# Performance work log

Hardware: AMD Instinct MI355X
Metric: run time of the kernel (lower is better)

## Reference

```python
import math
import jax, jax.numpy as jnp
import numpy as np

B, S, D, H = 4, 2048, 1024, 16
HD = D // H

def setup_inputs() -> dict:
    key = jax.random.key(0)
    ks = jax.random.split(key, 8)
    std = 1.0 / math.sqrt(D)
    return {
        "query": jax.random.normal(ks[0], (B, S, D), jnp.float32),
        "key":   jax.random.normal(ks[1], (B, S, D), jnp.float32),
        "value": jax.random.normal(ks[2], (B, S, D), jnp.float32),
        "Wq": jax.random.normal(ks[3], (D, D), jnp.float32) * std,
        "Wk": jax.random.normal(ks[4], (D, D), jnp.float32) * std,
        "Wv": jax.random.normal(ks[5], (D, D), jnp.float32) * std,
        "Wo": jax.random.normal(ks[6], (D, D), jnp.float32) * std,
        "bo": jnp.zeros((D,), jnp.float32),
    }

def reference(query, key, value, Wq, Wk, Wv, Wo, bo):
    # Projections (bias-free, as in source)
    Q = query @ Wq   # [B,S,D]
    K = key   @ Wk
    V = value @ Wv
    # Split heads: [B,S,D] -> [B,H,S,HD]
    def split(x):
        return x.reshape(B, S, H, HD).transpose(0, 2, 1, 3)
    Qh, Kh, Vh = split(Q), split(K), split(V)
    # NOTE: source scales by sqrt(d_model), not sqrt(head_dim)
    scale = 1.0 / math.sqrt(D)
    scores = jnp.einsum("bhqd,bhkd->bhqk", Qh, Kh) * scale  # [B,H,S,S]
    attn = jax.nn.softmax(scores, axis=-1)
    out = jnp.einsum("bhqk,bhkd->bhqd", attn, Vh)           # [B,H,S,HD]
    out = out.transpose(0, 2, 1, 3).reshape(B, S, D)
    return out @ Wo + bo
```

## Files before the change

kernel.cpp:

```cpp
#include <hip/hip_runtime.h>
#include <hip/hip_bf16.h>
#include <stdint.h>

typedef short bf16x8 __attribute__((ext_vector_type(8)));
typedef float f32x4 __attribute__((ext_vector_type(4)));
typedef float f32x16 __attribute__((ext_vector_type(16)));
typedef unsigned int uint2v __attribute__((ext_vector_type(2)));
typedef unsigned short u16;

static const size_t SD = (size_t)8192 * 1024;
static const size_t DD = (size_t)1024 * 1024;

__device__ __forceinline__ u16 f2bf(float f) {
  unsigned int u = __builtin_bit_cast(unsigned int, f);
  u += 0x7fffu + ((u >> 16) & 1u);
  return (u16)(u >> 16);
}

__device__ __forceinline__ unsigned int cvt_pk_bf16(float a, float b) {
  unsigned int r;
  asm("v_cvt_pk_bf16_f32 %0, %1, %2" : "=v"(r) : "v"(a), "v"(b));
  return r;
}

__device__ __forceinline__ float exp2_hw(float x) {
  float r;
  asm("v_exp_f32 %0, %1" : "=v"(r) : "v"(x));
  return r;
}

__device__ __forceinline__ void async_copy16(const void* g, void* l) {
  __builtin_amdgcn_global_load_lds(
      (const __attribute__((address_space(1))) unsigned int*)g,
      (__attribute__((address_space(3))) unsigned int*)l, 16, 0, 0);
}

__device__ __forceinline__ void wb2() {
  asm volatile("s_waitcnt vmcnt(2)\ns_barrier" ::: "memory");
  __builtin_amdgcn_sched_barrier(0);
}
__device__ __forceinline__ void wb0() {
  asm volatile("s_waitcnt vmcnt(0)\ns_barrier" ::: "memory");
  __builtin_amdgcn_sched_barrier(0);
}

__global__ __launch_bounds__(256) void k_tcast4(const float* __restrict__ W0,
                                                const float* __restrict__ W1,
                                                const float* __restrict__ W2,
                                                const float* __restrict__ W3,
                                                u16* __restrict__ Wt) {
  __shared__ float tile[32][33];
  const int idx = blockIdx.x >> 10;
  const float* W = (idx == 0) ? W0 : (idx == 1) ? W1 : (idx == 2) ? W2 : W3;
  u16* dst = Wt + (size_t)idx * DD;
  const int inner = blockIdx.x & 1023;
  const int bk = inner & 31, bn = inner >> 5;
  const int tx = threadIdx.x & 31, ty = threadIdx.x >> 5;
#pragma unroll
  for (int yy = 0; yy < 32; yy += 8)
    tile[ty + yy][tx] = W[(size_t)(bk * 32 + ty + yy) * 1024 + bn * 32 + tx];
  __syncthreads();
#pragma unroll
  for (int yy = 0; yy < 32; yy += 8)
    dst[(size_t)(bn * 32 + ty + yy) * 1024 + bk * 32 + tx] = f2bf(tile[tx][ty + yy]);
}

__global__ __launch_bounds__(512, 4) void k_gemm_qkv(const float* __restrict__ qin,
                                                     const float* __restrict__ kin,
                                                     const float* __restrict__ vin,
                                                     const u16* __restrict__ Wt,
                                                     u16* __restrict__ Qp,
                                                     u16* __restrict__ Kp,
                                                     u16* __restrict__ Vp) {
  __shared__ __align__(16) u16 As[2][128 * 64];
  __shared__ __align__(16) u16 Bs[2][128 * 64];
  const int tid = threadIdx.x;
  const int w = tid >> 6, l = tid & 63;
  const int l15 = l & 15, g = l >> 4;
  const int rowc = l >> 3, uu = l & 7;
  const int wm = w >> 2, wn = w & 3;
  const int seg = blockIdx.x >> 9;
  const int inner = blockIdx.x & 511;
  const int mb = inner & 63, nb = inner >> 6;

  const float* A = (seg == 0) ? qin : (seg == 1) ? kin : vin;
  const u16* Bt = Wt + (size_t)seg * DD;
  u16* C = (seg == 0) ? Qp : (seg == 1) ? Kp : Vp;
  const float scale = (seg == 0) ? 0.04508422f : 1.0f;

  const int scol = (uu ^ rowc) << 3;
  const u16* bS = Bt + (size_t)(nb * 128 + 16 * w + rowc) * 1024 + scol;
  const float* aS = A + (size_t)(mb * 128 + 16 * w + rowc) * 1024 + uu * 8;

  auto stageB = [&](int buf) {
#pragma unroll
    for (int i = 0; i < 2; ++i)
      async_copy16(bS + (size_t)i * 8 * 1024, &Bs[buf][(2 * w + i) * 512]);
    bS += 64;
  };
  float4 ar[2][2];
  auto loadA = [&]() {
#pragma unroll
    for (int i = 0; i < 2; ++i) {
      ar[i][0] = *(const float4*)(aS + (size_t)i * 8 * 1024);
      ar[i][1] = *(const float4*)(aS + (size_t)i * 8 * 1024 + 4);
    }
    aS += 64;
  };
  auto writeA = [&](int buf) {
#pragma unroll
    for (int i = 0; i < 2; ++i) {
      unsigned int wd[4];
      wd[0] = cvt_pk_bf16(ar[i][0].x, ar[i][0].y);
      wd[1] = cvt_pk_bf16(ar[i][0].z, ar[i][0].w);
      wd[2] = cvt_pk_bf16(ar[i][1].x, ar[i][1].y);
      wd[3] = cvt_pk_bf16(ar[i][1].z, ar[i][1].w);
      const int row = 16 * w + 8 * i + rowc;
      *(int4*)&As[buf][row * 64 + scol] = *(const int4*)wd;
    }
  };

  f32x4 acc[4][2] = {};

  loadA();
  stageB(0);
  writeA(0);
  __syncthreads();

  for (int kt = 0; kt < 16; ++kt) {
    const int cur = kt & 1;
    if (kt < 15) { loadA(); stageB(cur ^ 1); }

#pragma unroll
    for (int kk = 0; kk < 2; ++kk) {
      bf16x8 af[4], bfr[2];
#pragma unroll
      for (int mi = 0; mi < 4; ++mi) {
        const int row = 64 * wm + 16 * mi + l15;
        const int ul = (4 * kk + g) ^ (row & 7);
        af[mi] = *(const bf16x8*)&As[cur][row * 64 + ul * 8];
      }
#pragma unroll
      for (int nt = 0; nt < 2; ++nt) {
        const int row = 32 * wn + 16 * nt + l15;
        const int ul = (4 * kk + g) ^ (row & 7);
        bfr[nt] = *(const bf16x8*)&Bs[cur][row * 64 + ul * 8];
      }
#pragma unroll
      for (int mi = 0; mi < 4; ++mi)
#pragma unroll
        for (int nt = 0; nt < 2; ++nt)
          acc[mi][nt] = __builtin_amdgcn_mfma_f32_16x16x32_bf16(af[mi], bfr[nt],
                                                                acc[mi][nt], 0, 0, 0);
    }

    if (kt < 15) {
      writeA(cur ^ 1);
      __syncthreads();
    }
  }

  if (seg != 2) {
#pragma unroll
    for (int mi = 0; mi < 4; ++mi)
#pragma unroll
      for (int nt = 0; nt < 2; ++nt) {
        const int colg = nb * 128 + 32 * wn + 16 * nt + l15;
#pragma unroll
        for (int r = 0; r < 4; ++r) {
          const int rowg = mb * 128 + 64 * wm + 16 * mi + 4 * g + r;
          C[(size_t)rowg * 1024 + colg] = f2bf(acc[mi][nt][r] * scale);
        }
      }
  } else {
#pragma unroll
    for (int mi = 0; mi < 4; ++mi)
#pragma unroll
      for (int nt = 0; nt < 2; ++nt) {
        const int colg = nb * 128 + 32 * wn + 16 * nt + l15;
        const int rowbase = mb * 128 + 64 * wm + 16 * mi + 4 * g;
        const int bb = rowbase >> 11, s = rowbase & 2047;
        const int hh = colg >> 6, d = colg & 63;
        u16 o4[4];
#pragma unroll
        for (int r = 0; r < 4; ++r) o4[r] = f2bf(acc[mi][nt][r]);
        *(int2*)&C[((size_t)(bb * 16 + hh) * 64 + d) * 2048 + s] = *(const int2*)o4;
      }
  }
}

__global__ __launch_bounds__(512, 4) void k_gemm(const u16* __restrict__ A,
                                                 const u16* __restrict__ Bt,
                                                 float* __restrict__ Cout,
                                                 const float* __restrict__ bias) {
  __shared__ __align__(16) u16 As[2][128 * 64];
  __shared__ __align__(16) u16 Bs[2][128 * 64];
  const int tid = threadIdx.x;
  const int w = tid >> 6, l = tid & 63;
  const int l15 = l & 15, g = l >> 4;
  const int rowc = l >> 3, uu = l & 7;
  const int wm = w >> 2, wn = w & 3;
  const int mb = blockIdx.x & 63, nb = blockIdx.x >> 6;

  const int scol = (uu ^ rowc) << 3;
  const u16* aS = A  + (size_t)(mb * 128 + 16 * w + rowc) * 1024 + scol;
  const u16* bS = Bt + (size_t)(nb * 128 + 16 * w + rowc) * 1024 + scol;

  auto stage = [&](int buf) {
#pragma unroll
    for (int i = 0; i < 2; ++i) {
      async_copy16(aS + (size_t)i * 8 * 1024, &As[buf][(2 * w + i) * 512]);
      async_copy16(bS + (size_t)i * 8 * 1024, &Bs[buf][(2 * w + i) * 512]);
    }
    aS += 64; bS += 64;
  };

  f32x4 acc[4][2] = {};

  stage(0);
  wb0();

  for (int kt = 0; kt < 16; ++kt) {
    const int cur = kt & 1;
    if (kt < 15) stage(cur ^ 1);

#pragma unroll
    for (int kk = 0; kk < 2; ++kk) {
      bf16x8 af[4], bfr[2];
#pragma unroll
      for (int mi = 0; mi < 4; ++mi) {
        const int row = 64 * wm + 16 * mi + l15;
        const int ul = (4 * kk + g) ^ (row & 7);
        af[mi] = *(const bf16x8*)&As[cur][row * 64 + ul * 8];
      }
#pragma unroll
      for (int nt = 0; nt < 2; ++nt) {
        const int row = 32 * wn + 16 * nt + l15;
        const int ul = (4 * kk + g) ^ (row & 7);
        bfr[nt] = *(const bf16x8*)&Bs[cur][row * 64 + ul * 8];
      }
#pragma unroll
      for (int mi = 0; mi < 4; ++mi)
#pragma unroll
        for (int nt = 0; nt < 2; ++nt)
          acc[mi][nt] = __builtin_amdgcn_mfma_f32_16x16x32_bf16(af[mi], bfr[nt],
                                                                acc[mi][nt], 0, 0, 0);
    }

    if (kt < 15) wb0();
  }

#pragma unroll
  for (int mi = 0; mi < 4; ++mi)
#pragma unroll
    for (int nt = 0; nt < 2; ++nt) {
      const int colg = nb * 128 + 32 * wn + 16 * nt + l15;
      const float bv = bias[colg];
#pragma unroll
      for (int r = 0; r < 4; ++r) {
        const int rowg = mb * 128 + 64 * wm + 16 * mi + 4 * g + r;
        Cout[(size_t)rowg * 1024 + colg] = acc[mi][nt][r] + bv;
      }
    }
}

__global__ __launch_bounds__(512, 4) void k_attn(const u16* __restrict__ Qp,
                                                 const u16* __restrict__ Kp,
                                                 const u16* __restrict__ Vt_g,
                                                 u16* __restrict__ ctx) {
  __shared__ __align__(16) u16 Ks[3][32 * 128];
  __shared__ __align__(16) u16 Vs[3][32 * 128];
  const int tid = threadIdx.x;
  const int w = tid >> 6, l = tid & 63;
  const int l31 = l & 31, h = l >> 5;

  const int bid = (blockIdx.x & 7) * 64 + (blockIdx.x >> 3);
  const int qb = bid & 7, hd = (bid >> 3) & 15, b = bid >> 7;

  const u16* Qb = Qp + (size_t)b * 2048 * 1024 + hd * 64;
  const u16* Kb = Kp + (size_t)b * 2048 * 1024 + hd * 64;
  const u16* Vb = Vt_g + ((size_t)(b * 16 + hd) * 64) * 2048;

  const int q = qb * 256 + w * 32 + l31;

  bf16x8 aq[4];
#pragma unroll
  for (int kk = 0; kk < 4; ++kk)
    aq[kk] = *(const bf16x8*)&Qb[(size_t)q * 1024 + 16 * kk + 8 * h];

  bf16x8 ones;
#pragma unroll
  for (int j = 0; j < 8; ++j) ones[j] = (short)0x3F80;

  f32x16 acc[2] = {};
  f32x16 accL = {};

  const int srow = w * 4 + (l >> 4);
  const int dp = ((l & 15) ^ (srow & 15)) * 8;
  const u16* kS = Kb + (size_t)(srow + 32 * (dp >> 6)) * 1024 + (dp & 63);
  const u16* vS = Vb + (size_t)(srow + 32 * (dp >> 6)) * 2048 + (dp & 63);

  auto stage = [&](int buf) {
    async_copy16(kS, &Ks[buf][w * 512]);
    async_copy16(vS, &Vs[buf][w * 512]);
    kS += 64 * 1024;
    vS += 64;
  };

  stage(0);
  stage(1);
  asm volatile("s_waitcnt vmcnt(2)\ns_barrier" ::: "memory");
  __builtin_amdgcn_sched_barrier(0);

  int cb = 0, sb = 2;
  for (int t = 0; t < 32; ++t) {
    if (t < 30) stage(sb);

    const u16* Kc = Ks[cb];
    const u16* Vc = Vs[cb];

    f32x16 sc[2] = {};
    __builtin_amdgcn_s_setprio(1);
#pragma unroll
    for (int kvt = 0; kvt < 2; ++kvt)
#pragma unroll
      for (int kk = 0; kk < 4; ++kk) {
        const int un = (8 * kvt + 2 * kk + h) ^ (l31 & 15);
        bf16x8 bk = *(const bf16x8*)&Kc[l31 * 128 + un * 8];
        sc[kvt] = __builtin_amdgcn_mfma_f32_32x32x16_bf16(bk, aq[kk], sc[kvt], 0, 0, 0);
      }
    __builtin_amdgcn_s_setprio(0);

#pragma unroll
    for (int kvt = 0; kvt < 2; ++kvt)
#pragma unroll
      for (int r = 0; r < 16; ++r) sc[kvt][r] = exp2_hw(sc[kvt][r]);

    bf16x8 pa[4];
#pragma unroll
    for (int kvt = 0; kvt < 2; ++kvt)
#pragma unroll
      for (int bb = 0; bb < 2; ++bb) {
        union { unsigned int wd[4]; bf16x8 v; } fr;
#pragma unroll
        for (int i = 0; i < 2; ++i) {
          const unsigned int x = cvt_pk_bf16(sc[kvt][8 * bb + 2 * i], sc[kvt][8 * bb + 2 * i + 1]);
          const unsigned int y = cvt_pk_bf16(sc[kvt][8 * bb + 4 + 2 * i], sc[kvt][8 * bb + 5 + 2 * i]);
          const uint2v sw = __builtin_amdgcn_permlane32_swap(x, y, false, false);
          fr.wd[i] = sw[0];
          fr.wd[i + 2] = sw[1];
        }
        pa[2 * kvt + bb] = fr.v;
      }

    __builtin_amdgcn_s_setprio(1);
#pragma unroll
    for (int dt = 0; dt < 2; ++dt)
#pragma unroll
      for (int kc = 0; kc < 4; ++kc) {
        const int un = (8 * dt + 2 * kc + h) ^ (l31 & 15);
        bf16x8 bv = *(const bf16x8*)&Vc[l31 * 128 + un * 8];
        acc[dt] = __builtin_amdgcn_mfma_f32_32x32x16_bf16(bv, pa[kc], acc[dt], 0, 0, 0);
      }
#pragma unroll
    for (int kc = 0; kc < 4; ++kc)
      accL = __builtin_amdgcn_mfma_f32_32x32x16_bf16(ones, pa[kc], accL, 0, 0, 0);
    __builtin_amdgcn_s_setprio(0);

    if (t < 30) wb2();
    else if (t == 30) wb0();

    cb = (cb == 2) ? 0 : cb + 1;
    sb = (sb == 2) ? 0 : sb + 1;
  }

  const float inv = 1.0f / accL[0];
  u16* ob = ctx + (size_t)b * 2048 * 1024 + (size_t)q * 1024 + hd * 64;
#pragma unroll
  for (int dt = 0; dt < 2; ++dt)
#pragma unroll
    for (int c = 0; c < 4; ++c) {
      unsigned int w2[2];
      w2[0] = cvt_pk_bf16(acc[dt][4 * c] * inv, acc[dt][4 * c + 1] * inv);
      w2[1] = cvt_pk_bf16(acc[dt][4 * c + 2] * inv, acc[dt][4 * c + 3] * inv);
      *(int2*)&ob[32 * dt + 8 * c + 4 * h] = *(const int2*)w2;
    }
}

extern "C" void kernel_launch(void* const* d_in, const int* in_sizes, int n_in,
                              void* d_out, int out_size, void* d_ws, size_t ws_size,
                              hipStream_t stream) {
  const float* q  = (const float*)d_in[0];
  const float* k  = (const float*)d_in[1];
  const float* v  = (const float*)d_in[2];
  const float* Wq = (const float*)d_in[3];
  const float* Wk = (const float*)d_in[4];
  const float* Wv = (const float*)d_in[5];
  const float* Wo = (const float*)d_in[6];
  const float* bo = (const float*)d_in[7];

  u16* Wqt = (u16*)d_ws;
  u16* Wot = Wqt + 3 * DD;
  u16* Qp  = Wqt + 4 * DD;
  u16* Kp  = Qp + SD;
  u16* Vp  = Kp + SD;
  u16* ctx = Vp + SD;

  k_tcast4<<<4096, 256, 0, stream>>>(Wq, Wk, Wv, Wo, Wqt);
  k_gemm_qkv<<<1536, 512, 0, stream>>>(q, k, v, Wqt, Qp, Kp, Vp);
  k_attn<<<512, 512, 0, stream>>>(Qp, Kp, Vp, ctx);
  k_gemm<<<512, 512, 0, stream>>>(ctx, Wot, (float*)d_out, bo);
}
```

Measured before the change: 190.6 us.

## Stage fp32 A tiles via async copies and convert to bf16 at fragment load

```diff
diff --git a/kernel.cpp b/kernel.cpp
--- a/kernel.cpp
+++ b/kernel.cpp
@@ -72,12 +72,11 @@
                                                      u16* __restrict__ Qp,
                                                      u16* __restrict__ Kp,
                                                      u16* __restrict__ Vp) {
-  __shared__ __align__(16) u16 As[2][128 * 64];
-  __shared__ __align__(16) u16 Bs[2][128 * 64];
+  __shared__ __align__(16) float Afs[2][128 * 32];
+  __shared__ __align__(16) u16  Bs[2][128 * 32];
   const int tid = threadIdx.x;
   const int w = tid >> 6, l = tid & 63;
   const int l15 = l & 15, g = l >> 4;
-  const int rowc = l >> 3, uu = l & 7;
   const int wm = w >> 2, wn = w & 3;
   const int seg = blockIdx.x >> 9;
   const int inner = blockIdx.x & 511;
@@ -88,76 +87,57 @@
   u16* C = (seg == 0) ? Qp : (seg == 1) ? Kp : Vp;
   const float scale = (seg == 0) ? 0.04508422f : 1.0f;
 
-  const int scol = (uu ^ rowc) << 3;
-  const u16* bS = Bt + (size_t)(nb * 128 + 16 * w + rowc) * 1024 + scol;
-  const float* aS = A + (size_t)(mb * 128 + 16 * w + rowc) * 1024 + uu * 8;
-
-  auto stageB = [&](int buf) {
-#pragma unroll
-    for (int i = 0; i < 2; ++i)
-      async_copy16(bS + (size_t)i * 8 * 1024, &Bs[buf][(2 * w + i) * 512]);
-    bS += 64;
+  const int acol = 4 * ((l & 7) ^ ((l >> 3) & 7));
+  const float* aS0 = A + (size_t)(mb * 128 + (2 * w) * 8 + (l >> 3)) * 1024 + acol;
+  const float* aS1 = A + (size_t)(mb * 128 + (2 * w + 1) * 8 + (l >> 3)) * 1024 + acol;
+  const int bcol = 8 * ((l & 3) ^ ((l >> 2) & 3));
+  const u16* bS = Bt + (size_t)(nb * 128 + w * 16 + (l >> 2)) * 1024 + bcol;
+
+  auto stage = [&](int buf) {
+    async_copy16(aS0, &Afs[buf][(2 * w) * 256]);
+    async_copy16(aS1, &Afs[buf][(2 * w + 1) * 256]);
+    async_copy16(bS, &Bs[buf][w * 512]);
+    aS0 += 32; aS1 += 32; bS += 32;
   };
-  float4 ar[2][2];
-  auto loadA = [&]() {
-#pragma unroll
-    for (int i = 0; i < 2; ++i) {
-      ar[i][0] = *(const float4*)(aS + (size_t)i * 8 * 1024);
-      ar[i][1] = *(const float4*)(aS + (size_t)i * 8 * 1024 + 4);
-    }
-    aS += 64;
-  };
-  auto writeA = [&](int buf) {
-#pragma unroll
-    for (int i = 0; i < 2; ++i) {
+
+  f32x4 acc[4][2] = {};
+
+  stage(0);
+  wb0();
+
+  for (int kt = 0; kt < 32; ++kt) {
+    const int cur = kt & 1;
+    if (kt < 31) stage(cur ^ 1);
+
+    bf16x8 af[4], bfr[2];
+#pragma unroll
+    for (int mi = 0; mi < 4; ++mi) {
+      const int row = 64 * wm + 16 * mi + l15;
+      const int p0 = row * 8 + ((2 * g) ^ (row & 7));
+      const int p1 = row * 8 + ((2 * g + 1) ^ (row & 7));
+      const float4 fa = *(const float4*)&Afs[cur][p0 * 4];
+      const float4 fb = *(const float4*)&Afs[cur][p1 * 4];
       unsigned int wd[4];
-      wd[0] = cvt_pk_bf16(ar[i][0].x, ar[i][0].y);
-      wd[1] = cvt_pk_bf16(ar[i][0].z, ar[i][0].w);
-      wd[2] = cvt_pk_bf16(ar[i][1].x, ar[i][1].y);
-      wd[3] = cvt_pk_bf16(ar[i][1].z, ar[i][1].w);
-      const int row = 16 * w + 8 * i + rowc;
-      *(int4*)&As[buf][row * 64 + scol] = *(const int4*)wd;
-    }
-  };
-
-  f32x4 acc[4][2] = {};
-
-  loadA();
-  stageB(0);
-  writeA(0);
-  __syncthreads();
-
-  for (int kt = 0; kt < 16; ++kt) {
-    const int cur = kt & 1;
-    if (kt < 15) { loadA(); stageB(cur ^ 1); }
-
-#pragma unroll
-    for (int kk = 0; kk < 2; ++kk) {
-      bf16x8 af[4], bfr[2];
-#pragma unroll
-      for (int mi = 0; mi < 4; ++mi) {
-        const int row = 64 * wm + 16 * mi + l15;
-        const int ul = (4 * kk + g) ^ (row & 7);
-        af[mi] = *(const bf16x8*)&As[cur][row * 64 + ul * 8];
-      }
-#pragma unroll
-      for (int nt = 0; nt < 2; ++nt) {
-        const int row = 32 * wn + 16 * nt + l15;
-        const int ul = (4 * kk + g) ^ (row & 7);
-        bfr[nt] = *(const bf16x8*)&Bs[cur][row * 64 + ul * 8];
-      }
-#pragma unroll
-      for (int mi = 0; mi < 4; ++mi)
-#pragma unroll
-        for (int nt = 0; nt < 2; ++nt)
-          acc[mi][nt] = __builtin_amdgcn_mfma_f32_16x16x32_bf16(af[mi], bfr[nt],
-                                                                acc[mi][nt], 0, 0, 0);
-    }
-
-    if (kt < 15) {
-      writeA(cur ^ 1);
-      __syncthreads();
-    }
+      wd[0] = cvt_pk_bf16(fa.x, fa.y);
+      wd[1] = cvt_pk_bf16(fa.z, fa.w);
+      wd[2] = cvt_pk_bf16(fb.x, fb.y);
+      wd[3] = cvt_pk_bf16(fb.z, fb.w);
+      af[mi] = *(const bf16x8*)wd;
+    }
+#pragma unroll
+    for (int nt = 0; nt < 2; ++nt) {
+      const int row = 32 * wn + 16 * nt + l15;
+      const int pb = row * 4 + (g ^ (row & 3));
+      bfr[nt] = *(const bf16x8*)&Bs[cur][pb * 8];
+    }
+#pragma unroll
+    for (int mi = 0; mi < 4; ++mi)
+#pragma unroll
+      for (int nt = 0; nt < 2; ++nt)
+        acc[mi][nt] = __builtin_amdgcn_mfma_f32_16x16x32_bf16(af[mi], bfr[nt],
+                                                              acc[mi][nt], 0, 0, 0);
+
+    if (kt < 31) wb0();
   }
 
   if (seg != 2) {
```

Measured after the change: 191.2 us. About the same (+0.3%).
